# Performance work log

Hardware: AMD Instinct MI355X
Metric: run time of the kernel (lower is better)

Reference implementation:

```python
import jax, jax.numpy as jnp
import numpy as np

D_MODEL = 1024
N_HEAD = 8
STRIDE = 8
HEAD_DIM = D_MODEL // N_HEAD
NEG_INF = jnp.float32(-1e30)  # stand-in for -inf, safe under softmax


def setup_inputs() -> dict:
    key = jax.random.key(0)
    ks = jax.random.split(key, 8)
    B, TGT, SRC = 2, 1024, 8192
    scale = 1.0 / np.sqrt(D_MODEL)
    return {
        "q": jax.random.normal(ks[0], (B, TGT, D_MODEL), jnp.float32),
        "k": jax.random.normal(ks[1], (B, SRC, D_MODEL), jnp.float32),
        "v": jax.random.normal(ks[2], (B, SRC, D_MODEL), jnp.float32),
        "Wq": jax.random.normal(ks[3], (D_MODEL, D_MODEL), jnp.float32) * scale,
        "bq": jnp.zeros((D_MODEL,), jnp.float32),
        "Wk": jax.random.normal(ks[4], (D_MODEL, D_MODEL), jnp.float32) * scale,
        "bk": jnp.zeros((D_MODEL,), jnp.float32),
        "Wv": jax.random.normal(ks[5], (D_MODEL, D_MODEL), jnp.float32) * scale,
        "bv": jnp.zeros((D_MODEL,), jnp.float32),
        "Wo": jax.random.normal(ks[6], (D_MODEL, D_MODEL), jnp.float32) * scale,
        "bo": jnp.zeros((D_MODEL,), jnp.float32),
    }


def _hepos_head_mask(src_len):
    # mask_h[h, j] True where position j is DISALLOWED for head h:
    # (j - h) % stride != 0. If a head would mask everything, unmask j=0
    # (matches the torch fallback; cannot happen when n_head <= stride... it
    # can when h >= stride? here h < n_head <= stride handled generically).
    src_idx = jnp.arange(src_len)  # [src]
    h_idx = jnp.arange(N_HEAD)[:, None]  # [H,1]
    m = ((src_idx[None, :] - h_idx) % STRIDE) != 0  # [H, src]
    all_masked = jnp.all(m, axis=-1, keepdims=True)  # [H,1]
    m = m.at[:, 0].set(jnp.where(all_masked[:, 0], False, m[:, 0]))
    return m


def reference(q, k, v, Wq, bq, Wk, bk, Wv, bv, Wo, bo):
    B, tgt_len, _ = q.shape
    src_len = k.shape[1]
    # projections (torch Linear: x @ W^T + b; here W stored as [d_in, d_out])
    Q = (q @ Wq + bq).reshape(B, tgt_len, N_HEAD, HEAD_DIM)
    K = (k @ Wk + bk).reshape(B, src_len, N_HEAD, HEAD_DIM)
    V = (v @ Wv + bv).reshape(B, src_len, N_HEAD, HEAD_DIM)
    # dense scores [B, H, tgt, src]
    scores = jnp.einsum('bthd,bshd->bhts', Q, K) / np.sqrt(HEAD_DIM)
    head_mask = _hepos_head_mask(src_len)  # [H, src], True -> disallowed
    scores = jnp.where(head_mask[None, :, None, :], NEG_INF, scores)
    attn = jax.nn.softmax(scores, axis=-1)
    out = jnp.einsum('bhts,bshd->bthd', attn, V).reshape(B, tgt_len, D_MODEL)
    return out @ Wo + bo
```

## Files before the change

### kernel.cpp

```cpp
#include <hip/hip_runtime.h>
#include <hip/hip_bf16.h>
#include <stdint.h>

#define DM 1024
#define HD 128
#define NH 8
#define NB 2
#define TGT 1024
#define SRC 8192
#define JPH 1024
#define LOG2E 1.4426950408889634f

typedef __attribute__((ext_vector_type(8))) short bf16x8;
typedef __attribute__((ext_vector_type(4))) float f32x4;

__device__ __forceinline__ unsigned short f2bf(float f) {
  __hip_bfloat16 h = __float2bfloat16(f);
  return __builtin_bit_cast(unsigned short, h);
}

__device__ __forceinline__ void gload_lds16(const void* g, void* l) {
  __builtin_amdgcn_global_load_lds(
      (const __attribute__((address_space(1))) unsigned int*)g,
      (__attribute__((address_space(3))) unsigned int*)l, 16, 0, 0);
}

__global__ __launch_bounds__(256) void wconv_kernel(
    const float* __restrict__ Wq, const float* __restrict__ Wk,
    const float* __restrict__ Wv, const float* __restrict__ Wo,
    unsigned short* __restrict__ WTout) {
  __shared__ float tile[64][65];
  const float* W = (blockIdx.z == 0) ? Wq : (blockIdx.z == 1) ? Wk
                   : (blockIdx.z == 2) ? Wv : Wo;
  unsigned short* WT = WTout + (size_t)blockIdx.z * DM * DM;
  const int k0 = blockIdx.x * 64, n0 = blockIdx.y * 64;
  const int tid = threadIdx.x;
  const int tr = tid >> 4, tc = (tid & 15) * 4;
  for (int it = 0; it < 4; ++it) {
    int r = tr + it * 16;
    float4 vv = *(const float4*)(&W[(size_t)(k0 + r) * DM + n0 + tc]);
    tile[r][tc] = vv.x; tile[r][tc + 1] = vv.y;
    tile[r][tc + 2] = vv.z; tile[r][tc + 3] = vv.w;
  }
  __syncthreads();
  for (int it = 0; it < 4; ++it) {
    int n = tr + it * 16;
    ushort4 o;
    o.x = f2bf(tile[tc + 0][n]); o.y = f2bf(tile[tc + 1][n]);
    o.z = f2bf(tile[tc + 2][n]); o.w = f2bf(tile[tc + 3][n]);
    *(ushort4*)(&WT[(size_t)(n0 + n) * DM + k0 + tc]) = o;
  }
}

__global__ __launch_bounds__(256, 3) void proj_fused_kernel(
    const float* __restrict__ q, const float* __restrict__ k,
    const float* __restrict__ v, const unsigned short* __restrict__ WTall,
    const float* __restrict__ bq, const float* __restrict__ bk,
    const float* __restrict__ bv, unsigned short* __restrict__ Qp,
    unsigned short* __restrict__ Kp, unsigned short* __restrict__ VpT) {
  __shared__ unsigned short Ab[2][64 * 64];
  __shared__ unsigned short Bb[2][128 * 64];
  const int tid = threadIdx.x, lane = tid & 63, w = tid >> 6;
  const int wm = w >> 1, wn = w & 1;
  const int l15 = lane & 15, l4 = lane >> 4;

  const int bid = blockIdx.x;
  const int mode = bid >> 8;
  const int sub = bid & 255;
  const float* Asrc;
  const unsigned short* WT;
  const float* bias;
  int nbase, bh = 0, Mtile;
  if (mode == 0) {
    Asrc = q; WT = WTall; bias = bq;
    Mtile = sub >> 3; nbase = (sub & 7) * 128;
  } else {
    bh = sub >> 4; Mtile = sub & 15;
    nbase = (bh & 7) * 128;
    if (mode == 1) { Asrc = k; WT = WTall + (size_t)DM * DM; bias = bk; }
    else           { Asrc = v; WT = WTall + (size_t)2 * DM * DM; bias = bv; }
  }

  const int ar = tid >> 2;
  const int ac = (tid & 3) * 16;
  size_t growA;
  if (mode == 0) growA = (size_t)(Mtile * 64 + ar);
  else growA = (size_t)(bh >> 3) * SRC + (size_t)(bh & 7) +
               8u * (size_t)(Mtile * 64 + ar);
  const float* aptr = &Asrc[growA * DM + ac];

  auto issueA = [&](int t, float4 (&R)[4]) {
    const float* src = aptr + t * 64;
#pragma unroll
    for (int i = 0; i < 4; ++i) R[i] = *(const float4*)(src + i * 4);
  };
  auto commitA = [&](float4 (&R)[4], int buf) {
    unsigned char* abase = (unsigned char*)Ab[buf] + ar * 128;
#pragma unroll
    for (int h = 0; h < 2; ++h) {
      bf16x8 pk;
      float4 x = R[h * 2], y = R[h * 2 + 1];
      pk[0] = (short)f2bf(x.x); pk[1] = (short)f2bf(x.y);
      pk[2] = (short)f2bf(x.z); pk[3] = (short)f2bf(x.w);
      pk[4] = (short)f2bf(y.x); pk[5] = (short)f2bf(y.y);
      pk[6] = (short)f2bf(y.z); pk[7] = (short)f2bf(y.w);
      int b0 = (ac * 2 + h * 16) ^ ((ar & 7) << 4);
      *(bf16x8*)(abase + b0) = pk;
    }
  };
  auto stageB = [&](int t, int buf) {
    const int kk0 = t * 64;
#pragma unroll
    for (int it = 0; it < 4; ++it) {
      int gi = w * 4 + it;
      int row = gi * 8 + (lane >> 3);
      const unsigned char* g =
          (const unsigned char*)&WT[(size_t)(nbase + row) * DM + kk0];
      g += ((lane & 7) * 16) ^ ((row & 7) << 4);
      gload_lds16(g, (unsigned char*)Bb[buf] + gi * 1024);
    }
  };

  f32x4 acc[2][4] = {};
  float4 aR0[4], aR1[4];

  stageB(0, 0);
  issueA(0, aR0);
  issueA(1, aR1);
  commitA(aR0, 0);
  asm volatile("s_waitcnt vmcnt(4) lgkmcnt(0)" ::: "memory");
  __builtin_amdgcn_s_barrier();
  __builtin_amdgcn_sched_barrier(0);

  auto body = [&](int T, int CUR, float4 (&RC)[4], float4 (&RN)[4]) {
    if (T + 1 < 16) stageB(T + 1, CUR ^ 1);
    if (T + 2 < 16) issueA(T + 2, RC);

    bf16x8 af[2][2], bfr[4][2];
#pragma unroll
    for (int kk = 0; kk < 2; ++kk) {
#pragma unroll
      for (int f = 0; f < 2; ++f) {
        int ra = wm * 32 + f * 16 + l15;
        int ka = (kk * 64 + l4 * 16) ^ ((ra & 7) << 4);
        af[f][kk] = *(const bf16x8*)((const unsigned char*)Ab[CUR] + ra * 128 + ka);
      }
#pragma unroll
      for (int g = 0; g < 4; ++g) {
        int rb = wn * 64 + g * 16 + l15;
        int kb = (kk * 64 + l4 * 16) ^ ((rb & 7) << 4);
        bfr[g][kk] = *(const bf16x8*)((const unsigned char*)Bb[CUR] + rb * 128 + kb);
      }
    }
#pragma unroll
    for (int kk = 0; kk < 2; ++kk)
#pragma unroll
      for (int f = 0; f < 2; ++f)
#pragma unroll
        for (int g = 0; g < 4; ++g)
          acc[f][g] = __builtin_amdgcn_mfma_f32_16x16x32_bf16(
              af[f][kk], bfr[g][kk], acc[f][g], 0, 0, 0);

    if (T + 1 < 16) commitA(RN, CUR ^ 1);

    if (T + 2 < 16)
      asm volatile("s_waitcnt vmcnt(4) lgkmcnt(0)" ::: "memory");
    else
      asm volatile("s_waitcnt vmcnt(0) lgkmcnt(0)" ::: "memory");
    __builtin_amdgcn_s_barrier();
    __builtin_amdgcn_sched_barrier(0);
  };

  for (int tt = 0; tt < 16; tt += 2) {
    body(tt, 0, aR0, aR1);
    body(tt + 1, 1, aR1, aR0);
  }

#pragma unroll
  for (int f = 0; f < 2; ++f) {
#pragma unroll
    for (int g = 0; g < 4; ++g) {
      const int mloc = wm * 32 + f * 16 + l4 * 4;
      const int nloc = wn * 64 + g * 16 + l15;
      const float bs = bias[nbase + nloc];
      if (mode == 2) {
        const int d = nloc;
        const int jp = Mtile * 64 + mloc;
        ushort4 o;
        o.x = f2bf(acc[f][g][0] + bs); o.y = f2bf(acc[f][g][1] + bs);
        o.z = f2bf(acc[f][g][2] + bs); o.w = f2bf(acc[f][g][3] + bs);
        *(ushort4*)(&VpT[((size_t)bh * HD + d) * JPH + jp]) = o;
      } else if (mode == 1) {
        for (int i = 0; i < 4; ++i) {
          int jp = Mtile * 64 + mloc + i;
          Kp[((size_t)bh * JPH + jp) * HD + nloc] = f2bf(acc[f][g][i] + bs);
        }
      } else {
        for (int i = 0; i < 4; ++i) {
          int mg = Mtile * 64 + mloc + i;
          int bb = mg >> 10, tt2 = mg & 1023;
          int ng = nbase + nloc;
          int h = ng >> 7, d = ng & 127;
          Qp[(((size_t)bb * NH + h) * TGT + tt2) * HD + d] =
              f2bf((acc[f][g][i] + bs) * 0.08838834764831845f);
        }
      }
    }
  }
}

__global__ __launch_bounds__(256) void attn_kernel(
    const unsigned short* __restrict__ Qp, const unsigned short* __restrict__ Kp,
    const unsigned short* __restrict__ VpT, unsigned short* __restrict__ O) {
  __shared__ unsigned short Klds[64 * 128];
  __shared__ unsigned short Vlds[128 * 64];
  __shared__ unsigned short Plds[4 * 16 * 64];
  const int tid = threadIdx.x, lane = tid & 63, w = tid >> 6;
  const int tq = blockIdx.x, bh = blockIdx.y;
  const int T0 = tq * 64 + w * 16;
  const int l15 = lane & 15, l4 = lane >> 4;

  bf16x8 qf[4];
  {
    const unsigned short* qrow = &Qp[((size_t)bh * TGT + T0 + l15) * HD];
    for (int kf = 0; kf < 4; ++kf)
      qf[kf] = *(const bf16x8*)(&qrow[kf * 32 + l4 * 8]);
  }

  f32x4 acc_o[8] = {};
  float m_run = -INFINITY, l_run = 0.f;

  const unsigned short* kbh = Kp + (size_t)bh * JPH * HD;
  const unsigned short* vbh = VpT + (size_t)bh * HD * JPH;

  for (int jt = 0; jt < 16; ++jt) {
    const int j0 = jt * 64;
    for (int it = 0; it < 4; ++it) {
      int rb = w * 16 + it * 4;
      int row = rb + l4;
      const unsigned char* g =
          (const unsigned char*)(kbh + (size_t)(j0 + row) * HD);
      g += (l15 * 16) ^ ((row & 7) << 4);
      gload_lds16(g, &Klds[rb * 128]);
    }
    for (int it = 0; it < 4; ++it) {
      int rb = w * 32 + it * 8;
      int d = rb + (lane >> 3);
      const unsigned char* g =
          (const unsigned char*)(vbh + (size_t)d * JPH + j0);
      g += ((lane & 7) * 16) ^ ((d & 7) << 4);
      gload_lds16(g, &Vlds[rb * 64]);
    }
    __syncthreads();

    f32x4 acc_s[4] = {};
    for (int jf = 0; jf < 4; ++jf) {
      const int j = jf * 16 + l15;
      for (int kf = 0; kf < 4; ++kf) {
        int byteoff = (j * 256 + (kf * 32 + l4 * 8) * 2) ^ ((j & 7) << 4);
        bf16x8 kfr = *(const bf16x8*)((const unsigned char*)Klds + byteoff);
        acc_s[jf] = __builtin_amdgcn_mfma_f32_16x16x32_bf16(
            kfr, qf[kf], acc_s[jf], 0, 0, 0);
      }
    }

    float pmax = -INFINITY;
    for (int jf = 0; jf < 4; ++jf)
      for (int i = 0; i < 4; ++i) pmax = fmaxf(pmax, acc_s[jf][i]);
    pmax = fmaxf(pmax, __shfl_xor(pmax, 16, 64));
    pmax = fmaxf(pmax, __shfl_xor(pmax, 32, 64));
    const float m_new = fmaxf(m_run, pmax);
    const float alpha = exp2f((m_run - m_new) * LOG2E);
    float psum = 0.f;
    for (int jf = 0; jf < 4; ++jf) {
      float p0 = exp2f((acc_s[jf][0] - m_new) * LOG2E);
      float p1 = exp2f((acc_s[jf][1] - m_new) * LOG2E);
      float p2 = exp2f((acc_s[jf][2] - m_new) * LOG2E);
      float p3 = exp2f((acc_s[jf][3] - m_new) * LOG2E);
      psum += (p0 + p1) + (p2 + p3);
      ushort4 pk;
      pk.x = f2bf(p0); pk.y = f2bf(p1); pk.z = f2bf(p2); pk.w = f2bf(p3);
      int byteoff = (w * 2048 + l15 * 128 + (jf * 16 + l4 * 4) * 2) ^ ((l15 & 7) << 4);
      *(ushort4*)((unsigned char*)Plds + byteoff) = pk;
    }
    psum += __shfl_xor(psum, 16, 64);
    psum += __shfl_xor(psum, 32, 64);
    l_run = l_run * alpha + psum;
    m_run = m_new;

    float alphar[4];
    for (int i = 0; i < 4; ++i)
      alphar[i] = __shfl(alpha, (lane & 48) | (l4 * 4 + i), 64);
    for (int df = 0; df < 8; ++df) {
      acc_o[df][0] *= alphar[0]; acc_o[df][1] *= alphar[1];
      acc_o[df][2] *= alphar[2]; acc_o[df][3] *= alphar[3];
    }

    for (int kf2 = 0; kf2 < 2; ++kf2) {
      int poff = (w * 2048 + l15 * 128 + (kf2 * 32 + l4 * 8) * 2) ^ ((l15 & 7) << 4);
      bf16x8 pf = *(const bf16x8*)((const unsigned char*)Plds + poff);
      for (int df = 0; df < 8; ++df) {
        int d = df * 16 + l15;
        int voff = (d * 128 + (kf2 * 32 + l4 * 8) * 2) ^ ((d & 7) << 4);
        bf16x8 vf = *(const bf16x8*)((const unsigned char*)Vlds + voff);
        acc_o[df] = __builtin_amdgcn_mfma_f32_16x16x32_bf16(
            pf, vf, acc_o[df], 0, 0, 0);
      }
    }
    __syncthreads();
  }

  const float li = 1.0f / l_run;
  float linv[4];
  for (int i = 0; i < 4; ++i)
    linv[i] = __shfl(li, (lane & 48) | (l4 * 4 + i), 64);

  const int b = bh >> 3, h = bh & 7;
  for (int df = 0; df < 8; ++df)
    for (int i = 0; i < 4; ++i) {
      int t = T0 + l4 * 4 + i;
      int d = df * 16 + l15;
      O[((size_t)b * TGT + t) * DM + h * HD + d] = f2bf(acc_o[df][i] * linv[i]);
    }
}

__global__ __launch_bounds__(256) void oproj_kernel(
    const unsigned short* __restrict__ Oin, const unsigned short* __restrict__ WoT,
    const float* __restrict__ bo, float* __restrict__ out) {
  __shared__ unsigned short Ab[2][128 * 64];
  __shared__ unsigned short Bb[2][128 * 64];
  const int tid = threadIdx.x, lane = tid & 63, w = tid >> 6;
  const int wm = w >> 1, wn = w & 1;
  const int n0 = blockIdx.x * 128, m0 = blockIdx.y * 128;
  const int l15 = lane & 15, l4 = lane >> 4;

  auto stage = [&](const unsigned short* src, int rbase, int t, unsigned short* lds) {
    const int kk0 = t * 64;
    for (int it = 0; it < 4; ++it) {
      int gi = w * 4 + it;
      int row = gi * 8 + (lane >> 3);
      const unsigned char* g =
          (const unsigned char*)&src[(size_t)(rbase + row) * DM + kk0];
      g += ((lane & 7) * 16) ^ ((row & 7) << 4);
      gload_lds16(g, (unsigned char*)lds + gi * 1024);
    }
  };

  f32x4 acc[4][4] = {};
  stage(Oin, m0, 0, Ab[0]);
  stage(WoT, n0, 0, Bb[0]);
  __syncthreads();

  for (int t = 0; t < 16; ++t) {
    const int cur = t & 1;
    if (t < 15) {
      stage(Oin, m0, t + 1, Ab[cur ^ 1]);
      stage(WoT, n0, t + 1, Bb[cur ^ 1]);
    }
    bf16x8 af[4][2], bfr[4][2];
    for (int f = 0; f < 4; ++f)
      for (int kk = 0; kk < 2; ++kk) {
        int ra = wm * 64 + f * 16 + l15;
        int ka = (kk * 64 + l4 * 16) ^ ((ra & 7) << 4);
        af[f][kk] = *(const bf16x8*)((const unsigned char*)Ab[cur] + ra * 128 + ka);
        int rb = wn * 64 + f * 16 + l15;
        int kb = (kk * 64 + l4 * 16) ^ ((rb & 7) << 4);
        bfr[f][kk] = *(const bf16x8*)((const unsigned char*)Bb[cur] + rb * 128 + kb);
      }
    for (int kk = 0; kk < 2; ++kk)
      for (int fm = 0; fm < 4; ++fm)
        for (int fn = 0; fn < 4; ++fn)
          acc[fm][fn] = __builtin_amdgcn_mfma_f32_16x16x32_bf16(
              af[fm][kk], bfr[fn][kk], acc[fm][fn], 0, 0, 0);
    __syncthreads();
  }

  for (int fm = 0; fm < 4; ++fm)
    for (int fn = 0; fn < 4; ++fn) {
      int nn = n0 + wn * 64 + fn * 16 + l15;
      float bs = bo[nn];
      for (int i = 0; i < 4; ++i) {
        int mm = m0 + wm * 64 + fm * 16 + l4 * 4 + i;
        out[(size_t)mm * DM + nn] = acc[fm][fn][i] + bs;
      }
    }
}

extern "C" void kernel_launch(void* const* d_in, const int* in_sizes, int n_in,
                              void* d_out, int out_size, void* d_ws,
                              size_t ws_size, hipStream_t stream) {
  const float* q  = (const float*)d_in[0];
  const float* k  = (const float*)d_in[1];
  const float* v  = (const float*)d_in[2];
  const float* Wq = (const float*)d_in[3];
  const float* bq = (const float*)d_in[4];
  const float* Wk = (const float*)d_in[5];
  const float* bk = (const float*)d_in[6];
  const float* Wv = (const float*)d_in[7];
  const float* bv = (const float*)d_in[8];
  const float* Wo = (const float*)d_in[9];
  const float* bo = (const float*)d_in[10];
  float* out = (float*)d_out;

  unsigned short* WT  = (unsigned short*)d_ws;
  unsigned short* Qp  = WT + (size_t)4 * DM * DM;
  unsigned short* Kp  = Qp + (size_t)2 * DM * DM;
  unsigned short* VpT = Kp + (size_t)2 * DM * DM;
  unsigned short* Obf = VpT + (size_t)2 * DM * DM;

  hipLaunchKernelGGL(wconv_kernel, dim3(16, 16, 4), dim3(256), 0, stream,
                     Wq, Wk, Wv, Wo, WT);
  hipLaunchKernelGGL(proj_fused_kernel, dim3(768), dim3(256), 0, stream,
                     q, k, v, WT, bq, bk, bv, Qp, Kp, VpT);
  hipLaunchKernelGGL(attn_kernel, dim3(16, 16), dim3(256), 0, stream,
                     Qp, Kp, VpT, Obf);
  hipLaunchKernelGGL(oproj_kernel, dim3(8, 16), dim3(256), 0, stream,
                     Obf, WT + (size_t)3 * DM * DM, bo, out);
}
```

Before: 105.0 us.

## Shrink projection tiles, remap blocks across XCDs, double-buffer attention K/V

The projection kernel's M tile is halved to 32 rows, so it launches twice as many blocks at higher occupancy, and block IDs are remapped so consecutive logical tiles land on the same XCD. The attention kernel gets double-buffered K/V LDS tiles that prefetch the next tile during compute, plus an XCD-aware block remap on a flattened grid. The output projection uses 64-row M tiles to double its block count. Each block now moves more data per flop and attention uses more LDS, which may lower residency.

After: 103.5 us. Within noise of the previous version (-1.4%).

```diff
diff --git a/kernel.cpp b/kernel.cpp
--- a/kernel.cpp
+++ b/kernel.cpp
@@ -52,21 +52,22 @@
   }
 }
 
-__global__ __launch_bounds__(256, 3) void proj_fused_kernel(
+__global__ __launch_bounds__(256, 4) void proj_fused_kernel(
     const float* __restrict__ q, const float* __restrict__ k,
     const float* __restrict__ v, const unsigned short* __restrict__ WTall,
     const float* __restrict__ bq, const float* __restrict__ bk,
     const float* __restrict__ bv, unsigned short* __restrict__ Qp,
     unsigned short* __restrict__ Kp, unsigned short* __restrict__ VpT) {
-  __shared__ unsigned short Ab[2][64 * 64];
+  __shared__ unsigned short Ab[2][32 * 64];
   __shared__ unsigned short Bb[2][128 * 64];
   const int tid = threadIdx.x, lane = tid & 63, w = tid >> 6;
   const int wm = w >> 1, wn = w & 1;
   const int l15 = lane & 15, l4 = lane >> 4;
 
   const int bid = blockIdx.x;
-  const int mode = bid >> 8;
-  const int sub = bid & 255;
+  const int lbid = (bid & 7) * 192 + (bid >> 3);
+  const int mode = lbid >> 9;
+  const int sub = lbid & 511;
   const float* Asrc;
   const unsigned short* WT;
   const float* bias;
@@ -75,38 +76,33 @@
     Asrc = q; WT = WTall; bias = bq;
     Mtile = sub >> 3; nbase = (sub & 7) * 128;
   } else {
-    bh = sub >> 4; Mtile = sub & 15;
+    bh = sub >> 5; Mtile = sub & 31;
     nbase = (bh & 7) * 128;
     if (mode == 1) { Asrc = k; WT = WTall + (size_t)DM * DM; bias = bk; }
     else           { Asrc = v; WT = WTall + (size_t)2 * DM * DM; bias = bv; }
   }
 
-  const int ar = tid >> 2;
-  const int ac = (tid & 3) * 16;
+  const int ar = tid >> 3;
+  const int ac = (tid & 7) * 8;
   size_t growA;
-  if (mode == 0) growA = (size_t)(Mtile * 64 + ar);
+  if (mode == 0) growA = (size_t)(Mtile * 32 + ar);
   else growA = (size_t)(bh >> 3) * SRC + (size_t)(bh & 7) +
-               8u * (size_t)(Mtile * 64 + ar);
+               8u * (size_t)(Mtile * 32 + ar);
   const float* aptr = &Asrc[growA * DM + ac];
 
-  auto issueA = [&](int t, float4 (&R)[4]) {
+  auto issueA = [&](int t, float4 (&R)[2]) {
     const float* src = aptr + t * 64;
-#pragma unroll
-    for (int i = 0; i < 4; ++i) R[i] = *(const float4*)(src + i * 4);
-  };
-  auto commitA = [&](float4 (&R)[4], int buf) {
-    unsigned char* abase = (unsigned char*)Ab[buf] + ar * 128;
-#pragma unroll
-    for (int h = 0; h < 2; ++h) {
-      bf16x8 pk;
-      float4 x = R[h * 2], y = R[h * 2 + 1];
-      pk[0] = (short)f2bf(x.x); pk[1] = (short)f2bf(x.y);
-      pk[2] = (short)f2bf(x.z); pk[3] = (short)f2bf(x.w);
-      pk[4] = (short)f2bf(y.x); pk[5] = (short)f2bf(y.y);
-      pk[6] = (short)f2bf(y.z); pk[7] = (short)f2bf(y.w);
-      int b0 = (ac * 2 + h * 16) ^ ((ar & 7) << 4);
-      *(bf16x8*)(abase + b0) = pk;
-    }
+    R[0] = *(const float4*)(src);
+    R[1] = *(const float4*)(src + 4);
+  };
+  auto commitA = [&](float4 (&R)[2], int buf) {
+    bf16x8 pk;
+    pk[0] = (short)f2bf(R[0].x); pk[1] = (short)f2bf(R[0].y);
+    pk[2] = (short)f2bf(R[0].z); pk[3] = (short)f2bf(R[0].w);
+    pk[4] = (short)f2bf(R[1].x); pk[5] = (short)f2bf(R[1].y);
+    pk[6] = (short)f2bf(R[1].z); pk[7] = (short)f2bf(R[1].w);
+    int b0 = ar * 128 + ((ac * 2) ^ ((ar & 7) << 4));
+    *(bf16x8*)((unsigned char*)Ab[buf] + b0) = pk;
   };
   auto stageB = [&](int t, int buf) {
     const int kk0 = t * 64;
@@ -121,30 +117,27 @@
     }
   };
 
-  f32x4 acc[2][4] = {};
-  float4 aR0[4], aR1[4];
+  f32x4 acc[4] = {};
+  float4 aR0[2], aR1[2];
 
   stageB(0, 0);
   issueA(0, aR0);
+  commitA(aR0, 0);
   issueA(1, aR1);
-  commitA(aR0, 0);
-  asm volatile("s_waitcnt vmcnt(4) lgkmcnt(0)" ::: "memory");
+  asm volatile("s_waitcnt vmcnt(2) lgkmcnt(0)" ::: "memory");
   __builtin_amdgcn_s_barrier();
   __builtin_amdgcn_sched_barrier(0);
 
-  auto body = [&](int T, int CUR, float4 (&RC)[4], float4 (&RN)[4]) {
+  auto body = [&](int T, int CUR, float4 (&RC)[2], float4 (&RN)[2]) {
     if (T + 1 < 16) stageB(T + 1, CUR ^ 1);
     if (T + 2 < 16) issueA(T + 2, RC);
 
-    bf16x8 af[2][2], bfr[4][2];
+    bf16x8 af[2], bfr[4][2];
 #pragma unroll
     for (int kk = 0; kk < 2; ++kk) {
-#pragma unroll
-      for (int f = 0; f < 2; ++f) {
-        int ra = wm * 32 + f * 16 + l15;
-        int ka = (kk * 64 + l4 * 16) ^ ((ra & 7) << 4);
-        af[f][kk] = *(const bf16x8*)((const unsigned char*)Ab[CUR] + ra * 128 + ka);
-      }
+      int ra = wm * 16 + l15;
+      int ka = (kk * 64 + l4 * 16) ^ ((ra & 7) << 4);
+      af[kk] = *(const bf16x8*)((const unsigned char*)Ab[CUR] + ra * 128 + ka);
 #pragma unroll
       for (int g = 0; g < 4; ++g) {
         int rb = wn * 64 + g * 16 + l15;
@@ -155,16 +148,14 @@
 #pragma unroll
     for (int kk = 0; kk < 2; ++kk)
 #pragma unroll
-      for (int f = 0; f < 2; ++f)
-#pragma unroll
-        for (int g = 0; g < 4; ++g)
-          acc[f][g] = __builtin_amdgcn_mfma_f32_16x16x32_bf16(
-              af[f][kk], bfr[g][kk], acc[f][g], 0, 0, 0);
+      for (int g = 0; g < 4; ++g)
+        acc[g] = __builtin_amdgcn_mfma_f32_16x16x32_bf16(
+            af[kk], bfr[g][kk], acc[g], 0, 0, 0);
 
     if (T + 1 < 16) commitA(RN, CUR ^ 1);
 
     if (T + 2 < 16)
-      asm volatile("s_waitcnt vmcnt(4) lgkmcnt(0)" ::: "memory");
+      asm volatile("s_waitcnt vmcnt(2) lgkmcnt(0)" ::: "memory");
     else
       asm volatile("s_waitcnt vmcnt(0) lgkmcnt(0)" ::: "memory");
     __builtin_amdgcn_s_barrier();
@@ -177,33 +168,30 @@
   }
 
 #pragma unroll
-  for (int f = 0; f < 2; ++f) {
-#pragma unroll
-    for (int g = 0; g < 4; ++g) {
-      const int mloc = wm * 32 + f * 16 + l4 * 4;
-      const int nloc = wn * 64 + g * 16 + l15;
-      const float bs = bias[nbase + nloc];
-      if (mode == 2) {
-        const int d = nloc;
-        const int jp = Mtile * 64 + mloc;
-        ushort4 o;
-        o.x = f2bf(acc[f][g][0] + bs); o.y = f2bf(acc[f][g][1] + bs);
-        o.z = f2bf(acc[f][g][2] + bs); o.w = f2bf(acc[f][g][3] + bs);
-        *(ushort4*)(&VpT[((size_t)bh * HD + d) * JPH + jp]) = o;
-      } else if (mode == 1) {
-        for (int i = 0; i < 4; ++i) {
-          int jp = Mtile * 64 + mloc + i;
-          Kp[((size_t)bh * JPH + jp) * HD + nloc] = f2bf(acc[f][g][i] + bs);
-        }
-      } else {
-        for (int i = 0; i < 4; ++i) {
-          int mg = Mtile * 64 + mloc + i;
-          int bb = mg >> 10, tt2 = mg & 1023;
-          int ng = nbase + nloc;
-          int h = ng >> 7, d = ng & 127;
-          Qp[(((size_t)bb * NH + h) * TGT + tt2) * HD + d] =
-              f2bf((acc[f][g][i] + bs) * 0.08838834764831845f);
-        }
+  for (int g = 0; g < 4; ++g) {
+    const int mloc = wm * 16 + l4 * 4;
+    const int nloc = wn * 64 + g * 16 + l15;
+    const float bs = bias[nbase + nloc];
+    if (mode == 2) {
+      const int d = nloc;
+      const int jp = Mtile * 32 + mloc;
+      ushort4 o;
+      o.x = f2bf(acc[g][0] + bs); o.y = f2bf(acc[g][1] + bs);
+      o.z = f2bf(acc[g][2] + bs); o.w = f2bf(acc[g][3] + bs);
+      *(ushort4*)(&VpT[((size_t)bh * HD + d) * JPH + jp]) = o;
+    } else if (mode == 1) {
+      for (int i = 0; i < 4; ++i) {
+        int jp = Mtile * 32 + mloc + i;
+        Kp[((size_t)bh * JPH + jp) * HD + nloc] = f2bf(acc[g][i] + bs);
+      }
+    } else {
+      for (int i = 0; i < 4; ++i) {
+        int mg = Mtile * 32 + mloc + i;
+        int bb = mg >> 10, tt2 = mg & 1023;
+        int ng = nbase + nloc;
+        int h = ng >> 7, d = ng & 127;
+        Qp[(((size_t)bb * NH + h) * TGT + tt2) * HD + d] =
+            f2bf((acc[g][i] + bs) * 0.08838834764831845f);
       }
     }
   }
@@ -212,11 +200,13 @@
 __global__ __launch_bounds__(256) void attn_kernel(
     const unsigned short* __restrict__ Qp, const unsigned short* __restrict__ Kp,
     const unsigned short* __restrict__ VpT, unsigned short* __restrict__ O) {
-  __shared__ unsigned short Klds[64 * 128];
-  __shared__ unsigned short Vlds[128 * 64];
+  __shared__ unsigned short Klds[2][64 * 128];
+  __shared__ unsigned short Vlds[2][128 * 64];
   __shared__ unsigned short Plds[4 * 16 * 64];
   const int tid = threadIdx.x, lane = tid & 63, w = tid >> 6;
-  const int tq = blockIdx.x, bh = blockIdx.y;
+  const int bid = blockIdx.x;
+  const int lbid = (bid & 7) * 32 + (bid >> 3);
+  const int tq = lbid & 15, bh = lbid >> 4;
   const int T0 = tq * 64 + w * 16;
   const int l15 = lane & 15, l4 = lane >> 4;
 
@@ -233,32 +223,43 @@
   const unsigned short* kbh = Kp + (size_t)bh * JPH * HD;
   const unsigned short* vbh = VpT + (size_t)bh * HD * JPH;
 
-  for (int jt = 0; jt < 16; ++jt) {
+  auto stage = [&](int jt, int buf) {
     const int j0 = jt * 64;
+#pragma unroll
     for (int it = 0; it < 4; ++it) {
       int rb = w * 16 + it * 4;
       int row = rb + l4;
       const unsigned char* g =
           (const unsigned char*)(kbh + (size_t)(j0 + row) * HD);
       g += (l15 * 16) ^ ((row & 7) << 4);
-      gload_lds16(g, &Klds[rb * 128]);
-    }
+      gload_lds16(g, &Klds[buf][rb * 128]);
+    }
+#pragma unroll
     for (int it = 0; it < 4; ++it) {
       int rb = w * 32 + it * 8;
       int d = rb + (lane >> 3);
       const unsigned char* g =
           (const unsigned char*)(vbh + (size_t)d * JPH + j0);
       g += ((lane & 7) * 16) ^ ((d & 7) << 4);
-      gload_lds16(g, &Vlds[rb * 64]);
-    }
-    __syncthreads();
+      gload_lds16(g, &Vlds[buf][rb * 64]);
+    }
+  };
+
+  stage(0, 0);
+  asm volatile("s_waitcnt vmcnt(0)" ::: "memory");
+  __builtin_amdgcn_s_barrier();
+  __builtin_amdgcn_sched_barrier(0);
+
+  for (int jt = 0; jt < 16; ++jt) {
+    const int cb = jt & 1;
+    if (jt < 15) stage(jt + 1, cb ^ 1);
 
     f32x4 acc_s[4] = {};
     for (int jf = 0; jf < 4; ++jf) {
       const int j = jf * 16 + l15;
       for (int kf = 0; kf < 4; ++kf) {
         int byteoff = (j * 256 + (kf * 32 + l4 * 8) * 2) ^ ((j & 7) << 4);
-        bf16x8 kfr = *(const bf16x8*)((const unsigned char*)Klds + byteoff);
+        bf16x8 kfr = *(const bf16x8*)((const unsigned char*)Klds[cb] + byteoff);
         acc_s[jf] = __builtin_amdgcn_mfma_f32_16x16x32_bf16(
             kfr, qf[kf], acc_s[jf], 0, 0, 0);
       }
@@ -302,12 +303,15 @@
       for (int df = 0; df < 8; ++df) {
         int d = df * 16 + l15;
         int voff = (d * 128 + (kf2 * 32 + l4 * 8) * 2) ^ ((d & 7) << 4);
-        bf16x8 vf = *(const bf16x8*)((const unsigned char*)Vlds + voff);
+        bf16x8 vf = *(const bf16x8*)((const unsigned char*)Vlds[cb] + voff);
         acc_o[df] = __builtin_amdgcn_mfma_f32_16x16x32_bf16(
             pf, vf, acc_o[df], 0, 0, 0);
       }
     }
-    __syncthreads();
+
+    asm volatile("s_waitcnt vmcnt(0)" ::: "memory");
+    __builtin_amdgcn_s_barrier();
+    __builtin_amdgcn_sched_barrier(0);
   }
 
   const float li = 1.0f / l_run;
@@ -327,61 +331,88 @@
 __global__ __launch_bounds__(256) void oproj_kernel(
     const unsigned short* __restrict__ Oin, const unsigned short* __restrict__ WoT,
     const float* __restrict__ bo, float* __restrict__ out) {
-  __shared__ unsigned short Ab[2][128 * 64];
+  __shared__ unsigned short Ab[2][64 * 64];
   __shared__ unsigned short Bb[2][128 * 64];
   const int tid = threadIdx.x, lane = tid & 63, w = tid >> 6;
   const int wm = w >> 1, wn = w & 1;
-  const int n0 = blockIdx.x * 128, m0 = blockIdx.y * 128;
+  const int n0 = blockIdx.x * 128, m0 = blockIdx.y * 64;
   const int l15 = lane & 15, l4 = lane >> 4;
 
-  auto stage = [&](const unsigned short* src, int rbase, int t, unsigned short* lds) {
+  auto stageA = [&](int t, int buf) {
     const int kk0 = t * 64;
+#pragma unroll
+    for (int it = 0; it < 2; ++it) {
+      int gi = w * 2 + it;
+      int row = gi * 8 + (lane >> 3);
+      const unsigned char* g =
+          (const unsigned char*)&Oin[(size_t)(m0 + row) * DM + kk0];
+      g += ((lane & 7) * 16) ^ ((row & 7) << 4);
+      gload_lds16(g, (unsigned char*)Ab[buf] + gi * 1024);
+    }
+  };
+  auto stageB = [&](int t, int buf) {
+    const int kk0 = t * 64;
+#pragma unroll
     for (int it = 0; it < 4; ++it) {
       int gi = w * 4 + it;
       int row = gi * 8 + (lane >> 3);
       const unsigned char* g =
-          (const unsigned char*)&src[(size_t)(rbase + row) * DM + kk0];
+          (const unsigned char*)&WoT[(size_t)(n0 + row) * DM + kk0];
       g += ((lane & 7) * 16) ^ ((row & 7) << 4);
-      gload_lds16(g, (unsigned char*)lds + gi * 1024);
-    }
-  };
-
-  f32x4 acc[4][4] = {};
-  stage(Oin, m0, 0, Ab[0]);
-  stage(WoT, n0, 0, Bb[0]);
-  __syncthreads();
+      gload_lds16(g, (unsigned char*)Bb[buf] + gi * 1024);
+    }
+  };
+
+  f32x4 acc[2][4] = {};
+  stageA(0, 0);
+  stageB(0, 0);
+  asm volatile("s_waitcnt vmcnt(0)" ::: "memory");
+  __builtin_amdgcn_s_barrier();
+  __builtin_amdgcn_sched_barrier(0);
 
   for (int t = 0; t < 16; ++t) {
     const int cur = t & 1;
-    if (t < 15) {
-      stage(Oin, m0, t + 1, Ab[cur ^ 1]);
-      stage(WoT, n0, t + 1, Bb[cur ^ 1]);
-    }
-    bf16x8 af[4][2], bfr[4][2];
-    for (int f = 0; f < 4; ++f)
-      for (int kk = 0; kk < 2; ++kk) {
-        int ra = wm * 64 + f * 16 + l15;
+    if (t < 15) { stageA(t + 1, cur ^ 1); stageB(t + 1, cur ^ 1); }
+
+    bf16x8 af[2][2], bfr[4][2];
+#pragma unroll
+    for (int kk = 0; kk < 2; ++kk) {
+#pragma unroll
+      for (int f = 0; f < 2; ++f) {
+        int ra = wm * 32 + f * 16 + l15;
         int ka = (kk * 64 + l4 * 16) ^ ((ra & 7) << 4);
         af[f][kk] = *(const bf16x8*)((const unsigned char*)Ab[cur] + ra * 128 + ka);
-        int rb = wn * 64 + f * 16 + l15;
+      }
+#pragma unroll
+      for (int g = 0; g < 4; ++g) {
+        int rb = wn * 64 + g * 16 + l15;
         int kb = (kk * 64 + l4 * 16) ^ ((rb & 7) << 4);
-        bfr[f][kk] = *(const bf16x8*)((const unsigned char*)Bb[cur] + rb * 128 + kb);
-      }
+        bfr[g][kk] = *(const bf16x8*)((const unsigned char*)Bb[cur] + rb * 128 + kb);
+      }
+    }
+#pragma unroll
     for (int kk = 0; kk < 2; ++kk)
-      for (int fm = 0; fm < 4; ++fm)
-        for (int fn = 0; fn < 4; ++fn)
-          acc[fm][fn] = __builtin_amdgcn_mfma_f32_16x16x32_bf16(
-              af[fm][kk], bfr[fn][kk], acc[fm][fn], 0, 0, 0);
-    __syncthreads();
-  }
-
-  for (int fm = 0; fm < 4; ++fm)
-    for (int fn = 0; fn < 4; ++fn) {
-      int nn = n0 + wn * 64 + fn * 16 + l15;
+#pragma unroll
+      for (int f = 0; f < 2; ++f)
+#pragma unroll
+        for (int g = 0; g < 4; ++g)
+          acc[f][g] = __builtin_amdgcn_mfma_f32_16x16x32_bf16(
+              af[f][kk], bfr[g][kk], acc[f][g], 0, 0, 0);
+
+    asm volatile("s_waitcnt vmcnt(0) lgkmcnt(0)" ::: "memory");
+    __builtin_amdgcn_s_barrier();
+    __builtin_amdgcn_sched_barrier(0);
+  }
+
+#pragma unroll
+  for (int f = 0; f < 2; ++f)
+#pragma unroll
+    for (int g = 0; g < 4; ++g) {
+      int nn = n0 + wn * 64 + g * 16 + l15;
       float bs = bo[nn];
       for (int i = 0; i < 4; ++i) {
-        int mm = m0 + wm * 64 + fm * 16 + l4 * 4 + i;
-        out[(size_t)mm * DM + nn] = acc[fm][fn][i] + bs;
+        int mm = m0 + wm * 32 + f * 16 + l4 * 4 + i;
+        out[(size_t)mm * DM + nn] = acc[f][g][i] + bs;
       }
     }
 }
@@ -410,10 +441,10 @@
 
   hipLaunchKernelGGL(wconv_kernel, dim3(16, 16, 4), dim3(256), 0, stream,
                      Wq, Wk, Wv, Wo, WT);
-  hipLaunchKernelGGL(proj_fused_kernel, dim3(768), dim3(256), 0, stream,
+  hipLaunchKernelGGL(proj_fused_kernel, dim3(1536), dim3(256), 0, stream,
                      q, k, v, WT, bq, bk, bv, Qp, Kp, VpT);
-  hipLaunchKernelGGL(attn_kernel, dim3(16, 16), dim3(256), 0, stream,
+  hipLaunchKernelGGL(attn_kernel, dim3(256), dim3(256), 0, stream,
                      Qp, Kp, VpT, Obf);
-  hipLaunchKernelGGL(oproj_kernel, dim3(8, 16), dim3(256), 0, stream,
+  hipLaunchKernelGGL(oproj_kernel, dim3(8, 32), dim3(256), 0, stream,
                      Obf, WT + (size_t)3 * DM * DM, bo, out);
 }
```
